# Kernel tuning notes

Measured on AMD Instinct MI355X. Metric: run time of the kernel, lower is better.

The kernel has to match this reference:

```python
import jax, jax.numpy as jnp
import numpy as np

N, D, E = 50000, 128, 600000
EPS = 1e-5  # LayerNorm eps (torch default)


def setup_inputs() -> dict:
    key = jax.random.key(0)
    ks = jax.random.split(key, 8)
    s = D ** -0.5
    return {
        "in_feat": jax.random.normal(ks[0], (N, D), dtype=jnp.float32),
        "edge_src": jax.random.randint(ks[1], (E,), 0, N),
        "edge_dst": jax.random.randint(ks[2], (E,), 0, N),
        "W1": jax.random.normal(ks[3], (D, D), dtype=jnp.float32) * s,
        "b1": jnp.zeros((D,), jnp.float32),
        "W2": jax.random.normal(ks[4], (D, D), dtype=jnp.float32) * s,
        "b2": jnp.zeros((D,), jnp.float32),
        "ln1_w": jnp.ones((D,), jnp.float32),
        "ln1_b": jnp.zeros((D,), jnp.float32),
        "ln2_w": jnp.ones((D,), jnp.float32),
        "ln2_b": jnp.zeros((D,), jnp.float32),
    }


def layer_norm(x, w, b):
    mu = jnp.mean(x, axis=-1, keepdims=True)
    var = jnp.var(x, axis=-1, keepdims=True)
    return (x - mu) * jax.lax.rsqrt(var + EPS) * w + b


def gcn_conv(x, W, b, src, dst, deg_inv_sqrt):
    # PyG GCNConv: linear transform, then D^-1/2 (A+I) D^-1/2 propagation, then bias
    h = x @ W  # [N, D]
    norm = deg_inv_sqrt[src] * deg_inv_sqrt[dst]  # [E]
    agg = jax.ops.segment_sum(h[src] * norm[:, None], dst, num_segments=N)
    agg = agg + (deg_inv_sqrt ** 2)[:, None] * h  # self-loop term handled analytically
    return agg + b


def reference(in_feat, W1, b1, W2, b2, ln1_w, ln1_b, ln2_w, ln2_b, edge_src, edge_dst):
    # degree with self-loops, computed on destination (PyG convention)
    deg = jax.ops.segment_sum(jnp.ones((E,), in_feat.dtype), edge_dst, num_segments=N) + 1.0
    dis = jax.lax.rsqrt(deg)
    h = gcn_conv(in_feat, W1, b1, edge_src, edge_dst, dis)
    ori = in_feat  # in_feats == h_feats -> residual uses original input
    ln_params = [(ln1_w, ln1_b), (ln2_w, ln2_b)]
    for i in range(2):  # prop_step - 1 iterations
        h = h + ori  # res=True, residual=1.0
        h = layer_norm(h, *ln_params[i])
        h = jax.nn.relu(h)  # dropout=0 -> identity
        h = gcn_conv(h, W2, b2, edge_src, edge_dst, dis)
    return h
```

## Files before the change

### kernel.cpp

```cpp
#include <hip/hip_runtime.h>
#include <hip/hip_bf16.h>

typedef unsigned short bf16_t;
typedef __attribute__((ext_vector_type(4))) float f32x4;
typedef __attribute__((ext_vector_type(8))) unsigned short us8;

__device__ __forceinline__ float bf2f(bf16_t u) {
  return __uint_as_float(((unsigned int)u) << 16);
}
__device__ __forceinline__ bf16_t f2bf(float f) {
  unsigned int u = __float_as_uint(f);
  return (bf16_t)((u + 0x7FFFu + ((u >> 16) & 1u)) >> 16);
}

__global__ void UnifiedGNN_56521769616171_kernel() {}


__global__ void gnn_zero(int* p, int n) {
  int i = blockIdx.x * 256 + threadIdx.x;
  if (i < n) p[i] = 0;
}

__global__ void gnn_count(const int* dst, int* counts, int e, int n) {
  int i = blockIdx.x * 256 + threadIdx.x;
  if (i < e) {
    int d = dst[i];
    if (d >= 0 && d < n) atomicAdd(&counts[d], 1);
  }
}

__global__ void gnn_scan1(const int* counts, int* row_ptr, int* partials, int n) {
  __shared__ int wsum[4];
  int tid = threadIdx.x;
  int base = blockIdx.x * 1024 + tid * 4;
  int a0 = 0, a1 = 0, a2 = 0, a3 = 0;
  if (base + 3 < n) {
    a0 = counts[base]; a1 = counts[base + 1];
    a2 = counts[base + 2]; a3 = counts[base + 3];
  } else if (base < n) {
    a0 = counts[base];
    if (base + 1 < n) a1 = counts[base + 1];
    if (base + 2 < n) a2 = counts[base + 2];
  }
  int s0 = a0, s1 = s0 + a1, s2 = s1 + a2, s3 = s2 + a3;
  int lane = tid & 63;
  int wv = tid >> 6;
  int incl = s3;
  for (int off = 1; off < 64; off <<= 1) {
    int t = __shfl_up(incl, off);
    if (lane >= off) incl += t;
  }
  if (lane == 63) wsum[wv] = incl;
  __syncthreads();
  int woff = 0;
  for (int j = 0; j < 4; j++)
    if (j < wv) woff += wsum[j];
  int excl = woff + incl - s3;
  if (base < n) {
    row_ptr[base] = excl;
    if (base + 1 < n) row_ptr[base + 1] = excl + s0;
    if (base + 2 < n) row_ptr[base + 2] = excl + s1;
    if (base + 3 < n) row_ptr[base + 3] = excl + s2;
  }
  if (tid == 255) partials[blockIdx.x] = wsum[0] + wsum[1] + wsum[2] + wsum[3];
}

__global__ void gnn_scan2(const int* partials, int* offsets, int nb,
                          int* row_ptr, int n, int etot) {
  int l = threadIdx.x;
  int v = 0;
  if (l < nb) v = partials[l];
  int orig = v;
  for (int off = 1; off < 64; off <<= 1) {
    int t = __shfl_up(v, off);
    if (l >= off) v += t;
  }
  offsets[l] = v - orig;
  if (l == 0) row_ptr[n] = etot;
}

__global__ void gnn_scan3(int* row_ptr, const int* offsets, int* cursor,
                          const int* counts, float* dis, int n) {
  int base = blockIdx.x * 1024 + threadIdx.x * 4;
  int off = offsets[blockIdx.x];
  for (int j = 0; j < 4; j++) {
    int i = base + j;
    if (i < n) {
      int rp = row_ptr[i] + off;
      row_ptr[i] = rp;
      cursor[i] = rp;
      dis[i] = rsqrtf((float)counts[i] + 1.0f);
    }
  }
}

__global__ void gnn_fill(const int* src, const int* dst, int* cursor,
                         int* csr, int e, int n) {
  int i = blockIdx.x * 256 + threadIdx.x;
  if (i < e) {
    int d = dst[i];
    if (d >= 0 && d < n) {
      int pos = atomicAdd(&cursor[d], 1);
      csr[pos] = src[i];
    }
  }
}

__global__ __launch_bounds__(256) void gnn_gemm(const void* Xv,
    const float* W, const float* dis, bf16_t* A, int n, int ntiles, int xfmt) {
  __shared__ __align__(16) bf16_t Wt[128 * 128];
  int tid = threadIdx.x;

  for (int j = tid; j < 2048; j += 256) {
    int c = j & 127;
    int kb = j >> 7;
    int k0 = kb << 3;
    us8 v;
#pragma unroll
    for (int i = 0; i < 8; i++) v[i] = f2bf(W[(size_t)(k0 + i) * 128 + c]);
    *(us8*)&Wt[c * 128 + ((kb ^ (c & 15)) << 3)] = v;
  }
  __syncthreads();

  int lane = tid & 63;
  int wid = tid >> 6;
  int l15 = lane & 15;
  int lk = lane >> 4;
  const bf16_t* Xb = (const bf16_t*)Xv;
  const float* Xf = (const float*)Xv;

  for (int t = blockIdx.x; t < ntiles; t += gridDim.x) {
    int rowbase = t * 64 + wid * 16;
    int arow = rowbase + l15;
    int arc = arow < n ? arow : (n - 1);

    f32x4 acc[8];
#pragma unroll
    for (int c = 0; c < 8; c++) {
      acc[c][0] = 0.0f; acc[c][1] = 0.0f; acc[c][2] = 0.0f; acc[c][3] = 0.0f;
    }

#pragma unroll
    for (int ks = 0; ks < 4; ks++) {
      int kb = ks * 4 + lk;
      us8 ah, al;
      if (xfmt == 0) {
        float4 a0 = *(const float4*)(Xf + (size_t)arc * 128 + kb * 8);
        float4 a1 = *(const float4*)(Xf + (size_t)arc * 128 + kb * 8 + 4);
        ah[0] = f2bf(a0.x); al[0] = f2bf(a0.x - bf2f(ah[0]));
        ah[1] = f2bf(a0.y); al[1] = f2bf(a0.y - bf2f(ah[1]));
        ah[2] = f2bf(a0.z); al[2] = f2bf(a0.z - bf2f(ah[2]));
        ah[3] = f2bf(a0.w); al[3] = f2bf(a0.w - bf2f(ah[3]));
        ah[4] = f2bf(a1.x); al[4] = f2bf(a1.x - bf2f(ah[4]));
        ah[5] = f2bf(a1.y); al[5] = f2bf(a1.y - bf2f(ah[5]));
        ah[6] = f2bf(a1.z); al[6] = f2bf(a1.z - bf2f(ah[6]));
        ah[7] = f2bf(a1.w); al[7] = f2bf(a1.w - bf2f(ah[7]));
      } else {
        ah = *(const us8*)(Xb + (size_t)arc * 128 + kb * 8);
      }
#pragma unroll
      for (int c = 0; c < 8; c++) {
        int col = c * 16 + l15;
        us8 bf = *(const us8*)&Wt[col * 128 + ((kb ^ l15) << 3)];
        asm volatile("s_nop 2\n\tv_mfma_f32_16x16x32_bf16 %0, %1, %2, %0"
                     : "+v"(acc[c]) : "v"(ah), "v"(bf));
      }
      if (xfmt == 0) {
#pragma unroll
        for (int c = 0; c < 8; c++) {
          int col = c * 16 + l15;
          us8 bf = *(const us8*)&Wt[col * 128 + ((kb ^ l15) << 3)];
          asm volatile("s_nop 2\n\tv_mfma_f32_16x16x32_bf16 %0, %1, %2, %0"
                       : "+v"(acc[c]) : "v"(al), "v"(bf));
        }
      }
    }
    asm volatile("s_nop 7\n\ts_nop 7"
                 : "+v"(acc[0]), "+v"(acc[1]), "+v"(acc[2]), "+v"(acc[3]),
                   "+v"(acc[4]), "+v"(acc[5]), "+v"(acc[6]), "+v"(acc[7]));

#pragma unroll
    for (int j = 0; j < 4; j++) {
      int row = rowbase + lk * 4 + j;
      if (row < n) {
        float dd = dis[row];
#pragma unroll
        for (int c = 0; c < 8; c++) {
          A[(size_t)row * 128 + c * 16 + l15] = f2bf(acc[c][j] * dd);
        }
      }
    }
  }
}

__global__ __launch_bounds__(256) void gnn_aggln(const bf16_t* A,
    const float* dis, const int* row_ptr, const int* csr, const float* bias,
    const float* ori, const float* lnw, const float* lnb,
    bf16_t* Bout, float* Fout, int n, int do_ln) {
  int wid = threadIdx.x >> 6;
  int lane = threadIdx.x & 63;
  int g = lane >> 4;
  int l16 = lane & 15;
  int row = blockIdx.x * 16 + wid * 4 + g;
  bool active = row < n;
  int rc = active ? row : (n - 1);
  int e0 = row_ptr[rc];
  int e1 = active ? row_ptr[rc + 1] : e0;
  const us8* Av8 = (const us8*)A;

  float ax[8];
#pragma unroll
  for (int i = 0; i < 8; i++) ax[i] = 0.0f;

  for (int e = e0; e < e1; e += 16) {
    int nv = e1 - e;
    if (nv > 16) nv = 16;
    int sv = csr[e + (l16 < nv ? l16 : 0)];
#pragma unroll
    for (int j = 0; j < 16; j++) {
      if (j >= nv) break;
      int s = __shfl(sv, (g << 4) + j);
      us8 v = Av8[(size_t)s * 16 + l16];
#pragma unroll
      for (int i = 0; i < 8; i++) ax[i] += bf2f(v[i]);
    }
  }
  us8 sv8 = Av8[(size_t)rc * 16 + l16];
#pragma unroll
  for (int i = 0; i < 8; i++) ax[i] += bf2f(sv8[i]);

  float dd = dis[rc];
  float4 bb0 = *(const float4*)(bias + l16 * 8);
  float4 bb1 = *(const float4*)(bias + l16 * 8 + 4);
  float h[8];
  h[0] = dd * ax[0] + bb0.x; h[1] = dd * ax[1] + bb0.y;
  h[2] = dd * ax[2] + bb0.z; h[3] = dd * ax[3] + bb0.w;
  h[4] = dd * ax[4] + bb1.x; h[5] = dd * ax[5] + bb1.y;
  h[6] = dd * ax[6] + bb1.z; h[7] = dd * ax[7] + bb1.w;

  if (do_ln) {
    float4 o0 = *(const float4*)(ori + (size_t)rc * 128 + l16 * 8);
    float4 o1 = *(const float4*)(ori + (size_t)rc * 128 + l16 * 8 + 4);
    float v[8];
    v[0] = h[0] + o0.x; v[1] = h[1] + o0.y; v[2] = h[2] + o0.z; v[3] = h[3] + o0.w;
    v[4] = h[4] + o1.x; v[5] = h[5] + o1.y; v[6] = h[6] + o1.z; v[7] = h[7] + o1.w;
    float s = 0.0f, sq = 0.0f;
#pragma unroll
    for (int i = 0; i < 8; i++) { s += v[i]; sq += v[i] * v[i]; }
    for (int off = 8; off >= 1; off >>= 1) {
      s += __shfl_xor(s, off);
      sq += __shfl_xor(sq, off);
    }
    float mu = s * (1.0f / 128.0f);
    float var = sq * (1.0f / 128.0f) - mu * mu;
    float inv = rsqrtf(var + 1e-5f);
    float4 w0 = *(const float4*)(lnw + l16 * 8);
    float4 w1 = *(const float4*)(lnw + l16 * 8 + 4);
    float4 c0 = *(const float4*)(lnb + l16 * 8);
    float4 c1 = *(const float4*)(lnb + l16 * 8 + 4);
    float wv[8] = {w0.x, w0.y, w0.z, w0.w, w1.x, w1.y, w1.z, w1.w};
    float cv[8] = {c0.x, c0.y, c0.z, c0.w, c1.x, c1.y, c1.z, c1.w};
    us8 o8;
#pragma unroll
    for (int i = 0; i < 8; i++) {
      float y = (v[i] - mu) * inv * wv[i] + cv[i];
      if (y < 0.0f) y = 0.0f;
      o8[i] = f2bf(y);
    }
    if (active) *(us8*)(Bout + (size_t)rc * 128 + l16 * 8) = o8;
  } else {
    if (active) {
      float4 f0 = make_float4(h[0], h[1], h[2], h[3]);
      float4 f1 = make_float4(h[4], h[5], h[6], h[7]);
      *(float4*)(Fout + (size_t)rc * 128 + l16 * 8) = f0;
      *(float4*)(Fout + (size_t)rc * 128 + l16 * 8 + 4) = f1;
    }
  }
}


extern "C" void kernel_launch(void* const* d_in, const int* in_sizes, int n_in,
                              void* d_out, int out_size, void* d_ws, size_t ws_size,
                              hipStream_t stream) {
  UnifiedGNN_56521769616171_kernel<<<1, 64, 0, stream>>>();

  int nI = (n_in > 0 && n_in <= 16) ? n_in : 11;
  long best = -1;
  int iFeat = 0;
  for (int i = 0; i < nI; i++)
    if ((long)in_sizes[i] > best) { best = in_sizes[i]; iFeat = i; }
  int iW[2], iV[6], iE[2];
  int nW = 0, nV = 0, nE = 0;
  for (int i = 0; i < nI; i++) {
    if (i == iFeat) continue;
    int s = in_sizes[i];
    if (s == 128 * 128) { if (nW < 2) iW[nW++] = i; }
    else if (s == 128)  { if (nV < 6) iV[nV++] = i; }
    else                { if (nE < 2) iE[nE++] = i; }
  }
  int aFeat = 0, aEs = 1, aEd = 2, aW1 = 3, aB1 = 4, aW2 = 5, aB2 = 6,
      aL1w = 7, aL1b = 8, aL2w = 9, aL2b = 10;
  if (nW == 2 && nV == 6 && nE == 2) {
    aFeat = iFeat;
    aEs = iE[0]; aEd = iE[1];
    aW1 = iW[0]; aW2 = iW[1];
    aB1 = iV[0]; aB2 = iV[1];
    aL1w = iV[2]; aL1b = iV[3]; aL2w = iV[4]; aL2b = iV[5];
  }

  int N = 50000;
  int E = 600000;
  if (in_sizes[aFeat] > 0 && (in_sizes[aFeat] % 128) == 0) N = in_sizes[aFeat] / 128;
  if (in_sizes[aEs] > 0) E = in_sizes[aEs];

  const float* in_feat = (const float*)d_in[aFeat];
  const int*   esrc    = (const int*)d_in[aEs];
  const int*   edst    = (const int*)d_in[aEd];
  const float* W1      = (const float*)d_in[aW1];
  const float* b1      = (const float*)d_in[aB1];
  const float* W2      = (const float*)d_in[aW2];
  const float* b2      = (const float*)d_in[aB2];
  const float* ln1w    = (const float*)d_in[aL1w];
  const float* ln1b    = (const float*)d_in[aL1b];
  const float* ln2w    = (const float*)d_in[aL2w];
  const float* ln2b    = (const float*)d_in[aL2b];

  char* base = (char*)d_ws;
  size_t off = 0;
  int* counts = (int*)(base + off);   off += ((size_t)N * 4 + 255) & ~(size_t)255;
  int* row_ptr = (int*)(base + off);  off += ((size_t)(N + 1) * 4 + 255) & ~(size_t)255;
  int* cursor = (int*)(base + off);   off += ((size_t)N * 4 + 255) & ~(size_t)255;
  int* partials = (int*)(base + off); off += 256;
  int* offsets = (int*)(base + off);  off += 256;
  float* dis = (float*)(base + off);  off += ((size_t)N * 4 + 255) & ~(size_t)255;
  int* csr = (int*)(base + off);      off += ((size_t)E * 4 + 255) & ~(size_t)255;
  bf16_t* A = (bf16_t*)(base + off);  off += ((size_t)N * 256 + 255) & ~(size_t)255;
  bf16_t* B = (bf16_t*)(base + off);  off += ((size_t)N * 256 + 255) & ~(size_t)255;

  int nb = (N + 1023) / 1024;
  int gN = (N + 255) / 256;
  int gE = (E + 255) / 256;
  int nt64 = (N + 63) / 64;
  int agg_grid = (N + 15) / 16;

  gnn_zero<<<gN, 256, 0, stream>>>(counts, N);
  gnn_count<<<gE, 256, 0, stream>>>(edst, counts, E, N);
  gnn_scan1<<<nb, 256, 0, stream>>>(counts, row_ptr, partials, N);
  gnn_scan2<<<1, 64, 0, stream>>>(partials, offsets, nb, row_ptr, N, E);
  gnn_scan3<<<nb, 256, 0, stream>>>(row_ptr, offsets, cursor, counts, dis, N);
  gnn_fill<<<gE, 256, 0, stream>>>(esrc, edst, cursor, csr, E, N);

  gnn_gemm<<<nt64, 256, 0, stream>>>(in_feat, W1, dis, A, N, nt64, 0);
  gnn_aggln<<<agg_grid, 256, 0, stream>>>(A, dis, row_ptr, csr, b1, in_feat,
                                          ln1w, ln1b, B, (float*)nullptr, N, 1);

  gnn_gemm<<<nt64, 256, 0, stream>>>(B, W2, dis, A, N, nt64, 1);
  gnn_aggln<<<agg_grid, 256, 0, stream>>>(A, dis, row_ptr, csr, b2, in_feat,
                                          ln2w, ln2b, B, (float*)nullptr, N, 1);

  gnn_gemm<<<nt64, 256, 0, stream>>>(B, W2, dis, A, N, nt64, 1);
  gnn_aggln<<<agg_grid, 256, 0, stream>>>(A, dis, row_ptr, csr, b2,
                                          (const float*)nullptr, (const float*)nullptr,
                                          (const float*)nullptr, (bf16_t*)nullptr,
                                          (float*)d_out, N, 0);
}
```

Before: 284.7 us.

## Pad CSR rows to multiples of 16 with a zero dummy row to batch gathers

The scan rounds each node's degree up to a multiple of 16. A new prefill kernel fills the padded CSR with index N, which points to an extra all-zero row appended to A, and row_ptr[n] now comes from the padded total. The aggregation loop drops its per-chunk tail checks and issues all 16 neighbour loads before accumulating, to expose more memory-level parallelism. In exchange it performs extra gathers of the cached zero row, adds a prefill kernel and a larger CSR buffer, and uses more registers for the 16 buffered vectors.

```diff
diff --git a/kernel.cpp b/kernel.cpp
--- a/kernel.cpp
+++ b/kernel.cpp
@@ -42,6 +42,8 @@
     if (base + 1 < n) a1 = counts[base + 1];
     if (base + 2 < n) a2 = counts[base + 2];
   }
+  a0 = (a0 + 15) & ~15; a1 = (a1 + 15) & ~15;
+  a2 = (a2 + 15) & ~15; a3 = (a3 + 15) & ~15;
   int s0 = a0, s1 = s0 + a1, s2 = s1 + a2, s3 = s2 + a3;
   int lane = tid & 63;
   int wv = tid >> 6;
@@ -66,7 +68,7 @@
 }
 
 __global__ void gnn_scan2(const int* partials, int* offsets, int nb,
-                          int* row_ptr, int n, int etot) {
+                          int* row_ptr, int n) {
   int l = threadIdx.x;
   int v = 0;
   if (l < nb) v = partials[l];
@@ -76,7 +78,8 @@
     if (l >= off) v += t;
   }
   offsets[l] = v - orig;
-  if (l == 0) row_ptr[n] = etot;
+  int tot = __shfl(v, nb - 1);
+  if (l == 0) row_ptr[n] = tot;
 }
 
 __global__ void gnn_scan3(int* row_ptr, const int* offsets, int* cursor,
@@ -92,6 +95,12 @@
       dis[i] = rsqrtf((float)counts[i] + 1.0f);
     }
   }
+}
+
+__global__ void gnn_prefill(int* csr, long total, int nzero, bf16_t* Azrow) {
+  long i = (long)blockIdx.x * 256 + threadIdx.x;
+  if (blockIdx.x == 0 && threadIdx.x < 64) ((unsigned int*)Azrow)[threadIdx.x] = 0u;
+  if (i < total) csr[i] = nzero;
 }
 
 __global__ void gnn_fill(const int* src, const int* dst, int* cursor,
@@ -213,16 +222,17 @@
   for (int i = 0; i < 8; i++) ax[i] = 0.0f;
 
   for (int e = e0; e < e1; e += 16) {
-    int nv = e1 - e;
-    if (nv > 16) nv = 16;
-    int sv = csr[e + (l16 < nv ? l16 : 0)];
+    int sv = csr[e + l16];
+    us8 vv[16];
 #pragma unroll
     for (int j = 0; j < 16; j++) {
-      if (j >= nv) break;
       int s = __shfl(sv, (g << 4) + j);
-      us8 v = Av8[(size_t)s * 16 + l16];
-#pragma unroll
-      for (int i = 0; i < 8; i++) ax[i] += bf2f(v[i]);
+      vv[j] = Av8[(size_t)s * 16 + l16];
+    }
+#pragma unroll
+    for (int j = 0; j < 16; j++) {
+#pragma unroll
+      for (int i = 0; i < 8; i++) ax[i] += bf2f(vv[j][i]);
     }
   }
   us8 sv8 = Av8[(size_t)rc * 16 + l16];
@@ -327,27 +337,30 @@
 
   char* base = (char*)d_ws;
   size_t off = 0;
+  long ptot = (long)E + 16L * N;
   int* counts = (int*)(base + off);   off += ((size_t)N * 4 + 255) & ~(size_t)255;
   int* row_ptr = (int*)(base + off);  off += ((size_t)(N + 1) * 4 + 255) & ~(size_t)255;
   int* cursor = (int*)(base + off);   off += ((size_t)N * 4 + 255) & ~(size_t)255;
   int* partials = (int*)(base + off); off += 256;
   int* offsets = (int*)(base + off);  off += 256;
   float* dis = (float*)(base + off);  off += ((size_t)N * 4 + 255) & ~(size_t)255;
-  int* csr = (int*)(base + off);      off += ((size_t)E * 4 + 255) & ~(size_t)255;
-  bf16_t* A = (bf16_t*)(base + off);  off += ((size_t)N * 256 + 255) & ~(size_t)255;
+  int* csr = (int*)(base + off);      off += ((size_t)ptot * 4 + 255) & ~(size_t)255;
+  bf16_t* A = (bf16_t*)(base + off);  off += ((size_t)(N + 1) * 256 + 255) & ~(size_t)255;
   bf16_t* B = (bf16_t*)(base + off);  off += ((size_t)N * 256 + 255) & ~(size_t)255;
 
   int nb = (N + 1023) / 1024;
   int gN = (N + 255) / 256;
   int gE = (E + 255) / 256;
+  int gP = (int)((ptot + 255) / 256);
   int nt64 = (N + 63) / 64;
   int agg_grid = (N + 15) / 16;
 
   gnn_zero<<<gN, 256, 0, stream>>>(counts, N);
   gnn_count<<<gE, 256, 0, stream>>>(edst, counts, E, N);
   gnn_scan1<<<nb, 256, 0, stream>>>(counts, row_ptr, partials, N);
-  gnn_scan2<<<1, 64, 0, stream>>>(partials, offsets, nb, row_ptr, N, E);
+  gnn_scan2<<<1, 64, 0, stream>>>(partials, offsets, nb, row_ptr, N);
   gnn_scan3<<<nb, 256, 0, stream>>>(row_ptr, offsets, cursor, counts, dis, N);
+  gnn_prefill<<<gP, 256, 0, stream>>>(csr, ptot, N, A + (size_t)N * 128);
   gnn_fill<<<gE, 256, 0, stream>>>(esrc, edst, cursor, csr, E, N);
 
   gnn_gemm<<<nt64, 256, 0, stream>>>(in_feat, W1, dis, A, N, nt64, 0);
```

Result: no change. 288.1 us (+1.2%).
